# Optimization experiments

Measured on AMD Instinct MI355X. Metric: run time of the kernel, lower is better.

The kernel has to match this reference:

```python
import jax, jax.numpy as jnp
import numpy as np

ITERATIONS = 20
EPS = 1e-9

def setup_inputs() -> dict:
    key = jax.random.key(0)
    x = jax.random.normal(key, (8192, 64, 64), dtype=jnp.float32)
    return {"x": x}

def reference(x):
    M = jnp.exp(x)
    def body(_, M):
        M = M / (jnp.sum(M, axis=-1, keepdims=True) + EPS)
        M = M / (jnp.sum(M, axis=-2, keepdims=True) + EPS)
        return M
    M = jax.lax.fori_loop(0, ITERATIONS, body, M)
    return M
```

## Files before the change

kernel.cpp:

```cpp
#include <hip/hip_runtime.h>

#define ITERS 20
#define EPS 1e-9f


template <int CTRL>
__device__ __forceinline__ float dpp_add(float x) {
    int yi = __builtin_amdgcn_update_dpp(0, __float_as_int(x), CTRL, 0xf, 0xf, true);
    return x + __int_as_float(yi);
}

__global__ __launch_bounds__(256, 4) void sinkhorn_kernel(
        const float* __restrict__ x, float* __restrict__ out, int nmat) {
    const int lane = threadIdx.x & 63;
    const int wave = threadIdx.x >> 6;
    const int mat  = blockIdx.x * 4 + wave;
    if (mat >= nmat) return;
    const int bi = lane >> 3;
    const int bj = lane & 7;

    const float4* __restrict__ xin = (const float4*)(x + (size_t)mat * 4096);

    float b[8][8];
    #pragma unroll
    for (int r = 0; r < 8; ++r) {
        float4 lo = xin[(8 * bi + r) * 16 + 2 * bj + 0];
        float4 hi = xin[(8 * bi + r) * 16 + 2 * bj + 1];
        b[r][0] = __expf(lo.x); b[r][1] = __expf(lo.y);
        b[r][2] = __expf(lo.z); b[r][3] = __expf(lo.w);
        b[r][4] = __expf(hi.x); b[r][5] = __expf(hi.y);
        b[r][6] = __expf(hi.z); b[r][7] = __expf(hi.w);
    }

    float uu[8], vv[8];
    #pragma unroll
    for (int i = 0; i < 8; ++i) { uu[i] = 1.0f; vv[i] = 1.0f; }

    for (int it = 0; it < ITERS; ++it) {
        float p[8];
        #pragma unroll
        for (int r = 0; r < 8; ++r) {
            float s = 0.0f;
            #pragma unroll
            for (int c = 0; c < 8; ++c) s = fmaf(b[r][c], vv[c], s);
            p[r] = s;
        }
        #pragma unroll
        for (int r = 0; r < 8; ++r) p[r] = dpp_add<0xB1>(p[r]);
        #pragma unroll
        for (int r = 0; r < 8; ++r) p[r] = dpp_add<0x4E>(p[r]);
        #pragma unroll
        for (int r = 0; r < 8; ++r) p[r] = dpp_add<0x141>(p[r]);
        #pragma unroll
        for (int r = 0; r < 8; ++r) {
            float S = fmaf(uu[r], p[r], EPS);
            uu[r] *= __builtin_amdgcn_rcpf(S);
        }

        float q[8];
        #pragma unroll
        for (int c = 0; c < 8; ++c) {
            float s = 0.0f;
            #pragma unroll
            for (int r = 0; r < 8; ++r) s = fmaf(b[r][c], uu[r], s);
            q[c] = s;
        }
        #pragma unroll
        for (int c = 0; c < 8; ++c) q[c] = dpp_add<0x128>(q[c]);
        #pragma unroll
        for (int c = 0; c < 8; ++c) q[c] += __shfl_xor(q[c], 16, 64);
        #pragma unroll
        for (int c = 0; c < 8; ++c) q[c] += __shfl_xor(q[c], 32, 64);
        #pragma unroll
        for (int c = 0; c < 8; ++c) {
            float T = fmaf(vv[c], q[c], EPS);
            vv[c] *= __builtin_amdgcn_rcpf(T);
        }
    }

    float4* __restrict__ o = (float4*)(out + (size_t)mat * 4096);
    #pragma unroll
    for (int r = 0; r < 8; ++r) {
        float ur = uu[r];
        float4 lo, hi;
        lo.x = b[r][0] * ur * vv[0]; lo.y = b[r][1] * ur * vv[1];
        lo.z = b[r][2] * ur * vv[2]; lo.w = b[r][3] * ur * vv[3];
        hi.x = b[r][4] * ur * vv[4]; hi.y = b[r][5] * ur * vv[5];
        hi.z = b[r][6] * ur * vv[6]; hi.w = b[r][7] * ur * vv[7];
        o[(8 * bi + r) * 16 + 2 * bj + 0] = lo;
        o[(8 * bi + r) * 16 + 2 * bj + 1] = hi;
    }
}

extern "C" void kernel_launch(void* const* d_in, const int* in_sizes, int n_in,
                              void* d_out, int out_size, void* d_ws, size_t ws_size,
                              hipStream_t stream) {
    const float* x = (const float*)d_in[0];
    float* out = (float*)d_out;
    const int nmat = in_sizes[0] / 4096;
    const int blocks = (nmat + 3) / 4;
    sinkhorn_kernel<<<blocks, 256, 0, stream>>>(x, out, nmat);
}
```

Baseline: 249.6 us.

## Store exp matrix as packed fp16 and use dot2 with permlane swap reductions

Converts the per-thread 8x8 exp(x) tile to packed half2 values, in both row-major and column-major copies. The row and column mat-vec products then use fdot2 with fp32 accumulation, which halves the multiply-add instruction count in the compute-bound Sinkhorn loop. The cross-row shuffles for the column sums are replaced with permlane16/32 swap builtins where available. The cost is fp16 rounding of the matrix and of the scaling vectors, which may break accuracy tolerance, and fp16 overflow if any input exceeds about 11.

```diff
diff --git a/kernel.cpp b/kernel.cpp
--- a/kernel.cpp
+++ b/kernel.cpp
@@ -3,11 +3,43 @@
 #define ITERS 20
 #define EPS 1e-9f
 
+typedef _Float16 half2_t __attribute__((ext_vector_type(2)));
+
+__device__ __forceinline__ half2_t pkrtz(float a, float b) {
+    return __builtin_bit_cast(half2_t, __builtin_amdgcn_cvt_pkrtz(a, b));
+}
 
 template <int CTRL>
 __device__ __forceinline__ float dpp_add(float x) {
     int yi = __builtin_amdgcn_update_dpp(0, __float_as_int(x), CTRL, 0xf, 0xf, true);
     return x + __int_as_float(yi);
+}
+
+__device__ __forceinline__ float swap16_add(float x) {
+#if __has_builtin(__builtin_amdgcn_permlane16_swap)
+    auto r = __builtin_amdgcn_permlane16_swap(__float_as_uint(x), __float_as_uint(x),
+                                              false, false);
+    return __uint_as_float(r[0]) + __uint_as_float(r[1]);
+#else
+    return x + __shfl_xor(x, 16, 64);
+#endif
+}
+__device__ __forceinline__ float swap32_add(float x) {
+#if __has_builtin(__builtin_amdgcn_permlane32_swap)
+    auto r = __builtin_amdgcn_permlane32_swap(__float_as_uint(x), __float_as_uint(x),
+                                              false, false);
+    return __uint_as_float(r[0]) + __uint_as_float(r[1]);
+#else
+    return x + __shfl_xor(x, 32, 64);
+#endif
+}
+
+__device__ __forceinline__ float fdot2(half2_t a, half2_t b, float c) {
+#if __has_builtin(__builtin_amdgcn_fdot2)
+    return __builtin_amdgcn_fdot2(a, b, c, false);
+#else
+    return fmaf((float)a.x, (float)b.x, fmaf((float)a.y, (float)b.y, c));
+#endif
 }
 
 __global__ __launch_bounds__(256, 4) void sinkhorn_kernel(
@@ -21,15 +53,26 @@
 
     const float4* __restrict__ xin = (const float4*)(x + (size_t)mat * 4096);
 
-    float b[8][8];
+    half2_t bc[8][4];
+    half2_t br[8][4];
     #pragma unroll
-    for (int r = 0; r < 8; ++r) {
-        float4 lo = xin[(8 * bi + r) * 16 + 2 * bj + 0];
-        float4 hi = xin[(8 * bi + r) * 16 + 2 * bj + 1];
-        b[r][0] = __expf(lo.x); b[r][1] = __expf(lo.y);
-        b[r][2] = __expf(lo.z); b[r][3] = __expf(lo.w);
-        b[r][4] = __expf(hi.x); b[r][5] = __expf(hi.y);
-        b[r][6] = __expf(hi.z); b[r][7] = __expf(hi.w);
+    for (int r2 = 0; r2 < 4; ++r2) {
+        float4 a0 = xin[(8 * bi + 2 * r2 + 0) * 16 + 2 * bj + 0];
+        float4 a1 = xin[(8 * bi + 2 * r2 + 0) * 16 + 2 * bj + 1];
+        float4 c0 = xin[(8 * bi + 2 * r2 + 1) * 16 + 2 * bj + 0];
+        float4 c1 = xin[(8 * bi + 2 * r2 + 1) * 16 + 2 * bj + 1];
+        float e0[8] = {__expf(a0.x), __expf(a0.y), __expf(a0.z), __expf(a0.w),
+                       __expf(a1.x), __expf(a1.y), __expf(a1.z), __expf(a1.w)};
+        float e1[8] = {__expf(c0.x), __expf(c0.y), __expf(c0.z), __expf(c0.w),
+                       __expf(c1.x), __expf(c1.y), __expf(c1.z), __expf(c1.w)};
+        #pragma unroll
+        for (int c2 = 0; c2 < 4; ++c2) {
+            bc[2 * r2 + 0][c2] = pkrtz(e0[2 * c2], e0[2 * c2 + 1]);
+            bc[2 * r2 + 1][c2] = pkrtz(e1[2 * c2], e1[2 * c2 + 1]);
+        }
+        #pragma unroll
+        for (int c = 0; c < 8; ++c)
+            br[c][r2] = pkrtz(e0[c], e1[c]);
     }
 
     float uu[8], vv[8];
@@ -37,12 +80,16 @@
     for (int i = 0; i < 8; ++i) { uu[i] = 1.0f; vv[i] = 1.0f; }
 
     for (int it = 0; it < ITERS; ++it) {
+        half2_t vvh[4];
+        #pragma unroll
+        for (int c2 = 0; c2 < 4; ++c2)
+            vvh[c2] = pkrtz(vv[2 * c2], vv[2 * c2 + 1]);
         float p[8];
         #pragma unroll
         for (int r = 0; r < 8; ++r) {
             float s = 0.0f;
             #pragma unroll
-            for (int c = 0; c < 8; ++c) s = fmaf(b[r][c], vv[c], s);
+            for (int c2 = 0; c2 < 4; ++c2) s = fdot2(bc[r][c2], vvh[c2], s);
             p[r] = s;
         }
         #pragma unroll
@@ -57,20 +104,24 @@
             uu[r] *= __builtin_amdgcn_rcpf(S);
         }
 
+        half2_t uuh[4];
+        #pragma unroll
+        for (int r2 = 0; r2 < 4; ++r2)
+            uuh[r2] = pkrtz(uu[2 * r2], uu[2 * r2 + 1]);
         float q[8];
         #pragma unroll
         for (int c = 0; c < 8; ++c) {
             float s = 0.0f;
             #pragma unroll
-            for (int r = 0; r < 8; ++r) s = fmaf(b[r][c], uu[r], s);
+            for (int r2 = 0; r2 < 4; ++r2) s = fdot2(br[c][r2], uuh[r2], s);
             q[c] = s;
         }
         #pragma unroll
         for (int c = 0; c < 8; ++c) q[c] = dpp_add<0x128>(q[c]);
         #pragma unroll
-        for (int c = 0; c < 8; ++c) q[c] += __shfl_xor(q[c], 16, 64);
+        for (int c = 0; c < 8; ++c) q[c] = swap16_add(q[c]);
         #pragma unroll
-        for (int c = 0; c < 8; ++c) q[c] += __shfl_xor(q[c], 32, 64);
+        for (int c = 0; c < 8; ++c) q[c] = swap32_add(q[c]);
         #pragma unroll
         for (int c = 0; c < 8; ++c) {
             float T = fmaf(vv[c], q[c], EPS);
@@ -83,10 +134,14 @@
     for (int r = 0; r < 8; ++r) {
         float ur = uu[r];
         float4 lo, hi;
-        lo.x = b[r][0] * ur * vv[0]; lo.y = b[r][1] * ur * vv[1];
-        lo.z = b[r][2] * ur * vv[2]; lo.w = b[r][3] * ur * vv[3];
-        hi.x = b[r][4] * ur * vv[4]; hi.y = b[r][5] * ur * vv[5];
-        hi.z = b[r][6] * ur * vv[6]; hi.w = b[r][7] * ur * vv[7];
+        lo.x = (float)bc[r][0].x * ur * vv[0];
+        lo.y = (float)bc[r][0].y * ur * vv[1];
+        lo.z = (float)bc[r][1].x * ur * vv[2];
+        lo.w = (float)bc[r][1].y * ur * vv[3];
+        hi.x = (float)bc[r][2].x * ur * vv[4];
+        hi.y = (float)bc[r][2].y * ur * vv[5];
+        hi.z = (float)bc[r][3].x * ur * vv[6];
+        hi.w = (float)bc[r][3].y * ur * vv[7];
         o[(8 * bi + r) * 16 + 2 * bj + 0] = lo;
         o[(8 * bi + r) * 16 + 2 * bj + 1] = hi;
     }
```

After: 252.1 us. About the same (+1.0%).
